# Optimization experiments

Measured on AMD Instinct MI355X. Metric: run time of the kernel, lower is better.

## Reference

```python
import jax, jax.numpy as jnp
import numpy as np

N = 100000      # nodes
E = 1600000     # edges (avg degree 16)
NFEAT = 16
HID = 64
OUT = 4
K = 3           # TAGConv hops
L = 4           # number of TAGConv layers


def setup_inputs() -> dict:
    key = jax.random.key(0)
    ks = jax.random.split(key, 6)
    x = jax.random.normal(ks[0], (N, NFEAT), dtype=jnp.float32)
    edge_index = jax.random.randint(ks[1], (2, E), 0, N, dtype=jnp.int64)
    # TAGConv has one (bias-free) linear per hop k=0..K, plus a per-layer bias.
    W0 = jax.random.normal(ks[2], (K + 1, NFEAT, HID), dtype=jnp.float32) * 0.1
    b0 = jnp.zeros((HID,), dtype=jnp.float32)
    Wh = jax.random.normal(ks[3], (L - 1, K + 1, HID, HID), dtype=jnp.float32) * 0.1
    bh = jnp.zeros((L - 1, HID), dtype=jnp.float32)
    fcW = jax.random.normal(ks[4], (HID, OUT), dtype=jnp.float32) * 0.1
    fcb = jnp.zeros((OUT,), dtype=jnp.float32)
    return dict(x=x, edge_index=edge_index, W0=W0, b0=b0, Wh=Wh, bh=bh, fcW=fcW, fcb=fcb)


def _gcn_norm(src, dst, num_nodes):
    # symmetric GCN normalization, no self-loops (PyG TAGConv default)
    ones = jnp.ones(src.shape, dtype=jnp.float32)
    deg = jax.ops.segment_sum(ones, dst, num_segments=num_nodes)
    dinv = jnp.where(deg > 0, 1.0 / jnp.sqrt(jnp.maximum(deg, 1e-12)), 0.0)
    return dinv[src] * dinv[dst]  # [E]


def _tag_conv(x, src, dst, norm, W, b):
    # out = sum_{k=0..K} (A_norm^k x) W_k + b
    out = x @ W[0]
    h = x
    for k in range(1, W.shape[0]):
        h = jax.ops.segment_sum(norm[:, None] * h[src], dst, num_segments=x.shape[0])
        out = out + h @ W[k]
    return out + b


def reference(x, edge_index, W0, b0, Wh, bh, fcW, fcb):
    src, dst = edge_index[0], edge_index[1]
    norm = _gcn_norm(src, dst, x.shape[0])
    h = jax.nn.relu(_tag_conv(x, src, dst, norm, W0, b0))  # conv0 (+relu, dropout=identity)
    for l in range(Wh.shape[0] - 1):  # middle convs with relu
        h = jax.nn.relu(_tag_conv(h, src, dst, norm, Wh[l], bh[l]))
    h = _tag_conv(h, src, dst, norm, Wh[-1], bh[-1])  # last conv, no relu
    return h @ fcW + fcb  # [N, OUT]
```

## Files before the change

### kernel.cpp

```cpp
#include <hip/hip_runtime.h>
#include <hip/hip_fp16.h>

constexpr int Nn   = 100000;
constexpr int Ne   = 1600000;
constexpr int NF   = 16;
constexpr int HID  = 64;
constexpr int NOUT = 4;

union H8 { float4 f4; __half h[8]; };
union H4 { float2 f2; __half h[4]; };


__global__ __launch_bounds__(256) void hist_kernel(const int* __restrict__ dst,
                                                   int* __restrict__ cnt,
                                                   int* __restrict__ rank) {
    int e = blockIdx.x * 256 + threadIdx.x;
    if (e < Ne) rank[e] = atomicAdd(&cnt[dst[e]], 1);
}

__global__ __launch_bounds__(256) void scan1_kernel(const int* __restrict__ cnt,
                                                    int* __restrict__ rowptr,
                                                    int* __restrict__ bsum) {
    __shared__ int lds[256];
    int t = threadIdx.x;
    int base = blockIdx.x * 1024 + t * 4;
    int v0 = (base + 0 < Nn) ? cnt[base + 0] : 0;
    int v1 = (base + 1 < Nn) ? cnt[base + 1] : 0;
    int v2 = (base + 2 < Nn) ? cnt[base + 2] : 0;
    int v3 = (base + 3 < Nn) ? cnt[base + 3] : 0;
    lds[t] = v0 + v1 + v2 + v3;
    __syncthreads();
    for (int off = 1; off < 256; off <<= 1) {
        int a = lds[t];
        int b = (t >= off) ? lds[t - off] : 0;
        __syncthreads();
        lds[t] = a + b;
        __syncthreads();
    }
    int excl = (t > 0) ? lds[t - 1] : 0;
    if (base + 0 < Nn) rowptr[base + 0] = excl;
    if (base + 1 < Nn) rowptr[base + 1] = excl + v0;
    if (base + 2 < Nn) rowptr[base + 2] = excl + v0 + v1;
    if (base + 3 < Nn) rowptr[base + 3] = excl + v0 + v1 + v2;
    if (t == 255) bsum[blockIdx.x] = lds[255];
}

__global__ __launch_bounds__(128) void scan2_kernel(int* __restrict__ bsum, int nb) {
    __shared__ int lds[128];
    int t = threadIdx.x;
    int v = (t < nb) ? bsum[t] : 0;
    lds[t] = v;
    __syncthreads();
    for (int off = 1; off < 128; off <<= 1) {
        int a = lds[t];
        int b = (t >= off) ? lds[t - off] : 0;
        __syncthreads();
        lds[t] = a + b;
        __syncthreads();
    }
    if (t < nb) bsum[t] = lds[t] - v;
}

__global__ __launch_bounds__(256) void scan3_kernel(const int* __restrict__ cnt,
                                                    int* __restrict__ rowptr,
                                                    const int* __restrict__ bsum,
                                                    float* __restrict__ dinv) {
    int i = blockIdx.x * 256 + threadIdx.x;
    if (i < Nn) {
        rowptr[i] += bsum[i >> 10];
        int c = cnt[i];
        dinv[i] = (c > 0) ? 1.0f / sqrtf((float)c) : 0.0f;
    }
    if (i == 0) rowptr[Nn] = Ne;
}

__global__ __launch_bounds__(256) void scatter_kernel(const int* __restrict__ src,
                                                      const int* __restrict__ dst,
                                                      const int* __restrict__ rowptr,
                                                      const int* __restrict__ rank,
                                                      const float* __restrict__ dinv,
                                                      int2* __restrict__ edge2) {
    int e = blockIdx.x * 256 + threadIdx.x;
    if (e < Ne) {
        int d = dst[e];
        int s = src[e];
        int p = rowptr[d] + rank[e];
        edge2[p] = make_int2(s, __float_as_int(dinv[s]));
    }
}

__global__ __launch_bounds__(256) void xcvt_kernel(const float* __restrict__ x,
                                                   __half* __restrict__ xh) {
    int i = blockIdx.x * 256 + threadIdx.x;
    if (i < Nn * NF / 4) {
        float4 v = reinterpret_cast<const float4*>(x)[i];
        H4 o;
        o.h[0] = __float2half(v.x);
        o.h[1] = __float2half(v.y);
        o.h[2] = __float2half(v.z);
        o.h[3] = __float2half(v.w);
        reinterpret_cast<float2*>(xh)[i] = o.f2;
    }
}


__global__ __launch_bounds__(256) void pull64h_kernel(const __half* __restrict__ hin,
                                                      const int* __restrict__ rowptr,
                                                      const int2* __restrict__ edge2,
                                                      const float* __restrict__ dinv,
                                                      __half* __restrict__ hout) {
    int lane = threadIdx.x & 63;
    int q  = lane & 3;
    int eo = (lane >> 2) & 3;
    int g  = lane >> 4;
    int n = blockIdx.x * 16 + (threadIdx.x >> 6) * 4 + g;
    if (n >= Nn) return;
    int r0 = rowptr[n];
    int r1 = rowptr[n + 1];
    float a[16];
#pragma unroll
    for (int j = 0; j < 16; ++j) a[j] = 0.f;
#pragma unroll 2
    for (int e = r0 + eo; e < r1; e += 4) {
        int2 ed = edge2[e];
        float w = __int_as_float(ed.y);
        const float4* rp = reinterpret_cast<const float4*>(hin + (size_t)ed.x * 64 + q * 16);
        H8 u0, u1;
        u0.f4 = rp[0];
        u1.f4 = rp[1];
#pragma unroll
        for (int j = 0; j < 8; ++j) a[j] += w * __half2float(u0.h[j]);
#pragma unroll
        for (int j = 0; j < 8; ++j) a[8 + j] += w * __half2float(u1.h[j]);
    }
#pragma unroll
    for (int off = 4; off <= 8; off <<= 1)
#pragma unroll
        for (int j = 0; j < 16; ++j) a[j] += __shfl_xor(a[j], off);
    if (eo == 0) {
        float dn = dinv[n];
        H8 o0, o1;
#pragma unroll
        for (int j = 0; j < 8; ++j) o0.h[j] = __float2half(a[j] * dn);
#pragma unroll
        for (int j = 0; j < 8; ++j) o1.h[j] = __float2half(a[8 + j] * dn);
        float4* op = reinterpret_cast<float4*>(hout + (size_t)n * 64 + q * 16);
        op[0] = o0.f4;
        op[1] = o1.f4;
    }
}

__global__ __launch_bounds__(256) void pull16h_kernel(const __half* __restrict__ hin,
                                                      const int* __restrict__ rowptr,
                                                      const int2* __restrict__ edge2,
                                                      const float* __restrict__ dinv,
                                                      __half* __restrict__ hout) {
    int lane = threadIdx.x & 63;
    int q  = lane & 1;
    int eo = (lane >> 1) & 3;
    int g  = lane >> 3;
    int n = blockIdx.x * 32 + (threadIdx.x >> 6) * 8 + g;
    if (n >= Nn) return;
    int r0 = rowptr[n];
    int r1 = rowptr[n + 1];
    float a[8];
#pragma unroll
    for (int j = 0; j < 8; ++j) a[j] = 0.f;
#pragma unroll 2
    for (int e = r0 + eo; e < r1; e += 4) {
        int2 ed = edge2[e];
        float w = __int_as_float(ed.y);
        H8 u;
        u.f4 = *reinterpret_cast<const float4*>(hin + (size_t)ed.x * 16 + q * 8);
#pragma unroll
        for (int j = 0; j < 8; ++j) a[j] += w * __half2float(u.h[j]);
    }
#pragma unroll
    for (int off = 2; off <= 4; off <<= 1)
#pragma unroll
        for (int j = 0; j < 8; ++j) a[j] += __shfl_xor(a[j], off);
    if (eo == 0) {
        float dn = dinv[n];
        H8 o;
#pragma unroll
        for (int j = 0; j < 8; ++j) o.h[j] = __float2half(a[j] * dn);
        *reinterpret_cast<float4*>(hout + (size_t)n * 16 + q * 8) = o.f4;
    }
}

template <int ADDBIAS>
__global__ __launch_bounds__(256) void pull4_kernel(const float* __restrict__ uin,
                                                    const float* __restrict__ gadd,
                                                    const int* __restrict__ rowptr,
                                                    const int2* __restrict__ edge2,
                                                    const float* __restrict__ dinv,
                                                    const float* __restrict__ beff,
                                                    float* __restrict__ out) {
    int lane = threadIdx.x & 63;
    int eo = lane & 15;
    int n = blockIdx.x * 16 + ((threadIdx.x >> 6) << 2) + (lane >> 4);
    if (n >= Nn) return;
    int r0 = rowptr[n];
    int r1 = rowptr[n + 1];
    float ax = 0.f, ay = 0.f, az = 0.f, aw = 0.f;
    for (int e = r0 + eo; e < r1; e += 16) {
        int2 ed = edge2[e];
        float w = __int_as_float(ed.y);
        float4 v = *reinterpret_cast<const float4*>(uin + (size_t)ed.x * 4);
        ax += w * v.x;
        ay += w * v.y;
        az += w * v.z;
        aw += w * v.w;
    }
#pragma unroll
    for (int off = 1; off < 16; off <<= 1) {
        ax += __shfl_xor(ax, off);
        ay += __shfl_xor(ay, off);
        az += __shfl_xor(az, off);
        aw += __shfl_xor(aw, off);
    }
    if (eo == 0) {
        float dn = dinv[n];
        float4 g = *reinterpret_cast<const float4*>(gadd + (size_t)n * 4);
        float4 o;
        o.x = g.x + dn * ax;
        o.y = g.y + dn * ay;
        o.z = g.z + dn * az;
        o.w = g.w + dn * aw;
        if (ADDBIAS) {
            o.x += beff[0]; o.y += beff[1]; o.z += beff[2]; o.w += beff[3];
        }
        *reinterpret_cast<float4*>(out + (size_t)n * 4) = o;
    }
}


template <int KS>
__global__ __launch_bounds__(256) void gemm4_kernel(const __half* __restrict__ S0,
                                                    const __half* __restrict__ S1,
                                                    const __half* __restrict__ S2,
                                                    const __half* __restrict__ S3,
                                                    const float* __restrict__ W,
                                                    const float* __restrict__ bias,
                                                    __half* __restrict__ out) {
    constexpr int PITCH = KS + 4;
    __shared__ float Ht[128 * PITCH];
    __shared__ float Wt[KS * 64];
    int t = threadIdx.x;
    int c4 = t & 15;
    int r8 = t >> 4;
    int r0 = blockIdx.x * 128;
    float acc[8][4];
#pragma unroll
    for (int j = 0; j < 8; ++j)
#pragma unroll
        for (int d = 0; d < 4; ++d) acc[j][d] = 0.f;

    const __half* Ss[4] = {S0, S1, S2, S3};
#pragma unroll
    for (int k = 0; k < 4; ++k) {
        const __half* S = Ss[k];
        for (int i = t; i < KS * 16; i += 256)
            *reinterpret_cast<float4*>(&Wt[i * 4]) =
                *reinterpret_cast<const float4*>(W + (size_t)k * KS * 64 + i * 4);
        for (int i = t; i < 128 * (KS / 8); i += 256) {
            int r = i / (KS / 8);
            int c8 = i % (KS / 8);
            int row = r0 + r;
            float* hp = &Ht[r * PITCH + c8 * 8];
            if (row < Nn) {
                H8 u;
                u.f4 = *reinterpret_cast<const float4*>(S + (size_t)row * KS + c8 * 8);
#pragma unroll
                for (int j = 0; j < 8; ++j) hp[j] = __half2float(u.h[j]);
            } else {
#pragma unroll
                for (int j = 0; j < 8; ++j) hp[j] = 0.f;
            }
        }
        __syncthreads();
#pragma unroll 4
        for (int f = 0; f < KS; ++f) {
            float4 b4 = *reinterpret_cast<const float4*>(&Wt[f * 64 + c4 * 4]);
#pragma unroll
            for (int j = 0; j < 8; ++j) {
                float a = Ht[(r8 + 16 * j) * PITCH + f];
                acc[j][0] += a * b4.x;
                acc[j][1] += a * b4.y;
                acc[j][2] += a * b4.z;
                acc[j][3] += a * b4.w;
            }
        }
        __syncthreads();
    }
    float4 bi = *reinterpret_cast<const float4*>(bias + c4 * 4);
#pragma unroll
    for (int j = 0; j < 8; ++j) {
        int row = r0 + r8 + 16 * j;
        if (row < Nn) {
            H4 o;
            o.h[0] = __float2half(fmaxf(acc[j][0] + bi.x, 0.f));
            o.h[1] = __float2half(fmaxf(acc[j][1] + bi.y, 0.f));
            o.h[2] = __float2half(fmaxf(acc[j][2] + bi.z, 0.f));
            o.h[3] = __float2half(fmaxf(acc[j][3] + bi.w, 0.f));
            *reinterpret_cast<float2*>(out + (size_t)row * 64 + c4 * 4) = o.f2;
        }
    }
}

__global__ __launch_bounds__(256) void weff_kernel(const float* __restrict__ W,
                                                   const float* __restrict__ b,
                                                   const float* __restrict__ fcW,
                                                   const float* __restrict__ fcb,
                                                   float* __restrict__ Wg,
                                                   float* __restrict__ beff) {
    int t = threadIdx.x;
    int k = t >> 6, c = t & 63;
    const float* wrow = W + (size_t)t * 64;
    float a0 = 0.f, a1 = 0.f, a2 = 0.f, a3 = 0.f;
    for (int d = 0; d < 64; ++d) {
        float w = wrow[d];
        a0 += w * fcW[d * 4 + 0];
        a1 += w * fcW[d * 4 + 1];
        a2 += w * fcW[d * 4 + 2];
        a3 += w * fcW[d * 4 + 3];
    }
    float4 o; o.x = a0; o.y = a1; o.z = a2; o.w = a3;
    *reinterpret_cast<float4*>(Wg + k * 256 + c * 4) = o;
    if (t < 4) {
        float s = fcb[t];
        for (int d = 0; d < 64; ++d) s += b[d] * fcW[d * 4 + t];
        beff[t] = s;
    }
}

__global__ __launch_bounds__(256) void gemmG_kernel(const __half* __restrict__ h,
                                                    const float* __restrict__ Wg,
                                                    float* __restrict__ G) {
    __shared__ float Ht[64 * 65];
    __shared__ float Wl[1024];
    int t = threadIdx.x;
    int r0 = blockIdx.x * 64;
    for (int i = t; i < 256; i += 256)
        *reinterpret_cast<float4*>(&Wl[i * 4]) = *reinterpret_cast<const float4*>(Wg + i * 4);
    for (int i = t; i < 64 * 8; i += 256) {
        int r = i >> 3;
        int c8 = i & 7;
        int row = r0 + r;
        float* hp = &Ht[r * 65 + c8 * 8];
        if (row < Nn) {
            H8 u;
            u.f4 = *reinterpret_cast<const float4*>(h + (size_t)row * 64 + c8 * 8);
#pragma unroll
            for (int j = 0; j < 8; ++j) hp[j] = __half2float(u.h[j]);
        } else {
#pragma unroll
            for (int j = 0; j < 8; ++j) hp[j] = 0.f;
        }
    }
    __syncthreads();
    int r = t & 63;
    int k = t >> 6;
    float a0 = 0.f, a1 = 0.f, a2 = 0.f, a3 = 0.f;
#pragma unroll 8
    for (int c = 0; c < 64; ++c) {
        float hv = Ht[r * 65 + c];
        const float* wp = &Wl[k * 256 + c * 4];
        a0 += hv * wp[0];
        a1 += hv * wp[1];
        a2 += hv * wp[2];
        a3 += hv * wp[3];
    }
    int row = r0 + r;
    if (row < Nn) {
        float4 o; o.x = a0; o.y = a1; o.z = a2; o.w = a3;
        *reinterpret_cast<float4*>(G + (size_t)k * Nn * 4 + (size_t)row * 4) = o;
    }
}


extern "C" void kernel_launch(void* const* d_in, const int* in_sizes, int n_in,
                              void* d_out, int out_size, void* d_ws, size_t ws_size,
                              hipStream_t stream) {
    const float* x   = (const float*)d_in[0];
    const int*   ei  = (const int*)d_in[1];
    const float* W0  = (const float*)d_in[2];
    const float* b0  = (const float*)d_in[3];
    const float* Wh  = (const float*)d_in[4];
    const float* bh  = (const float*)d_in[5];
    const float* fcW = (const float*)d_in[6];
    const float* fcb = (const float*)d_in[7];
    float* out = (float*)d_out;

    const int* src = ei;
    const int* dst = ei + Ne;

    int*    rowptr = (int*)d_ws;
    int2*   edge2  = (int2*)(rowptr + 100004);
    int*    rank   = (int*)(rowptr + 100004 + 2 * Ne);
    float*  dinv   = (float*)(rank + Ne);
    int*    bsum   = (int*)(dinv + Nn);
    float*  Wg     = (float*)(bsum + 128);
    float*  beff   = Wg + 1024;
    __half* xh     = (__half*)(beff + 16);
    __half* H0     = xh + (size_t)Nn * NF;
    __half* H1     = H0 + (size_t)Nn * HID;
    __half* H2     = H1 + (size_t)Nn * HID;
    __half* H3     = H2 + (size_t)Nn * HID;
    float*  G      = (float*)(H3 + (size_t)Nn * HID);
    float*  G0     = G + 0 * (size_t)Nn * 4;
    float*  G1     = G + 1 * (size_t)Nn * 4;
    float*  G2     = G + 2 * (size_t)Nn * 4;
    float*  G3     = G + 3 * (size_t)Nn * 4;
    float*  T      = G + 4 * (size_t)Nn * 4;
    float*  T2     = G + 5 * (size_t)Nn * 4;
    int*    cnt    = (int*)(T2 + (size_t)Nn * 4);

    const int egrid  = (Ne + 255) / 256;
    const int ngrid  = (Nn + 255) / 256;
    const int sgrid  = (Nn + 1023) / 1024;
    const int p64grid = (Nn + 15) / 16;
    const int p16grid = (Nn + 31) / 32;
    const int ggrid  = (Nn + 127) / 128;
    const int qgrid  = (Nn + 15) / 16;
    const int Ggrid  = (Nn + 63) / 64;
    const int cgrid  = (Nn * NF / 4 + 255) / 256;

    hipMemsetAsync(cnt, 0, Nn * sizeof(int), stream);
    hist_kernel<<<egrid, 256, 0, stream>>>(dst, cnt, rank);
    scan1_kernel<<<sgrid, 256, 0, stream>>>(cnt, rowptr, bsum);
    scan2_kernel<<<1, 128, 0, stream>>>(bsum, sgrid);
    scan3_kernel<<<ngrid, 256, 0, stream>>>(cnt, rowptr, bsum, dinv);
    scatter_kernel<<<egrid, 256, 0, stream>>>(src, dst, rowptr, rank, dinv, edge2);
    weff_kernel<<<1, 256, 0, stream>>>(Wh + 2 * 4 * 64 * 64, bh + 2 * 64, fcW, fcb, Wg, beff);
    xcvt_kernel<<<cgrid, 256, 0, stream>>>(x, xh);

    pull16h_kernel<<<p16grid, 256, 0, stream>>>(xh, rowptr, edge2, dinv, H1);
    pull16h_kernel<<<p16grid, 256, 0, stream>>>(H1, rowptr, edge2, dinv, H2);
    pull16h_kernel<<<p16grid, 256, 0, stream>>>(H2, rowptr, edge2, dinv, H3);
    gemm4_kernel<NF><<<ggrid, 256, 0, stream>>>(xh, H1, H2, H3, W0, b0, H0);

    for (int l = 0; l < 2; ++l) {
        pull64h_kernel<<<p64grid, 256, 0, stream>>>(H0, rowptr, edge2, dinv, H1);
        pull64h_kernel<<<p64grid, 256, 0, stream>>>(H1, rowptr, edge2, dinv, H2);
        pull64h_kernel<<<p64grid, 256, 0, stream>>>(H2, rowptr, edge2, dinv, H3);
        gemm4_kernel<HID><<<ggrid, 256, 0, stream>>>(H0, H1, H2, H3,
                                                     Wh + (size_t)l * 4 * HID * HID,
                                                     bh + (size_t)l * HID, H0);
    }

    gemmG_kernel<<<Ggrid, 256, 0, stream>>>(H0, Wg, G);
    pull4_kernel<0><<<qgrid, 256, 0, stream>>>(G3, G2, rowptr, edge2, dinv, beff, T);
    pull4_kernel<0><<<qgrid, 256, 0, stream>>>(T,  G1, rowptr, edge2, dinv, beff, T2);
    pull4_kernel<1><<<qgrid, 256, 0, stream>>>(T2, G0, rowptr, edge2, dinv, beff, out);
}
```

Before: 629.9 us.

## Replace atomic-rank CSR build with two-level bucketed counting sort

Builds the CSR by first bucketing edges by dst>>8 with per-chunk LDS histograms and a global scan, scattering (src,dst) pairs into buckets, then sorting each bucket locally in LDS to produce rowptr, dinv and column sources. This replaces the global per-node atomic histogram and the random scatter that used a rank array, aiming to cut global atomic contention and uncoalesced writes. It adds several kernels, extra passes over edge data and a staging buffer aliased onto H1/H2.

```diff
diff --git a/kernel.cpp b/kernel.cpp
--- a/kernel.cpp
+++ b/kernel.cpp
@@ -7,27 +7,39 @@
 constexpr int HID  = 64;
 constexpr int NOUT = 4;
 
+constexpr int NBUK  = 391;
+constexpr int CHUNK = 2048;
+constexpr int NB1   = (Ne + CHUNK - 1) / CHUNK;
+constexpr int NS    = NBUK * NB1;
+constexpr int STASH = 6144;
+
 union H8 { float4 f4; __half h[8]; };
 union H4 { float2 f2; __half h[4]; };
 
 
-__global__ __launch_bounds__(256) void hist_kernel(const int* __restrict__ dst,
-                                                   int* __restrict__ cnt,
-                                                   int* __restrict__ rank) {
-    int e = blockIdx.x * 256 + threadIdx.x;
-    if (e < Ne) rank[e] = atomicAdd(&cnt[dst[e]], 1);
-}
-
-__global__ __launch_bounds__(256) void scan1_kernel(const int* __restrict__ cnt,
-                                                    int* __restrict__ rowptr,
-                                                    int* __restrict__ bsum) {
+__global__ __launch_bounds__(256) void bhist_kernel(const int* __restrict__ dst,
+                                                    int* __restrict__ ghist) {
+    __shared__ int h[NBUK];
+    int t = threadIdx.x;
+    int b = blockIdx.x;
+    for (int i = t; i < NBUK; i += 256) h[i] = 0;
+    __syncthreads();
+    int e0 = b * CHUNK;
+    int e1 = (e0 + CHUNK < Ne) ? e0 + CHUNK : Ne;
+    for (int e = e0 + t; e < e1; e += 256) atomicAdd(&h[dst[e] >> 8], 1);
+    __syncthreads();
+    for (int i = t; i < NBUK; i += 256) ghist[i * NB1 + b] = h[i];
+}
+
+__global__ __launch_bounds__(256) void scan1g_kernel(int* __restrict__ g,
+                                                     int* __restrict__ bsum) {
     __shared__ int lds[256];
     int t = threadIdx.x;
     int base = blockIdx.x * 1024 + t * 4;
-    int v0 = (base + 0 < Nn) ? cnt[base + 0] : 0;
-    int v1 = (base + 1 < Nn) ? cnt[base + 1] : 0;
-    int v2 = (base + 2 < Nn) ? cnt[base + 2] : 0;
-    int v3 = (base + 3 < Nn) ? cnt[base + 3] : 0;
+    int v0 = (base + 0 < NS) ? g[base + 0] : 0;
+    int v1 = (base + 1 < NS) ? g[base + 1] : 0;
+    int v2 = (base + 2 < NS) ? g[base + 2] : 0;
+    int v3 = (base + 3 < NS) ? g[base + 3] : 0;
     lds[t] = v0 + v1 + v2 + v3;
     __syncthreads();
     for (int off = 1; off < 256; off <<= 1) {
@@ -38,20 +50,20 @@
         __syncthreads();
     }
     int excl = (t > 0) ? lds[t - 1] : 0;
-    if (base + 0 < Nn) rowptr[base + 0] = excl;
-    if (base + 1 < Nn) rowptr[base + 1] = excl + v0;
-    if (base + 2 < Nn) rowptr[base + 2] = excl + v0 + v1;
-    if (base + 3 < Nn) rowptr[base + 3] = excl + v0 + v1 + v2;
+    if (base + 0 < NS) g[base + 0] = excl;
+    if (base + 1 < NS) g[base + 1] = excl + v0;
+    if (base + 2 < NS) g[base + 2] = excl + v0 + v1;
+    if (base + 3 < NS) g[base + 3] = excl + v0 + v1 + v2;
     if (t == 255) bsum[blockIdx.x] = lds[255];
 }
 
-__global__ __launch_bounds__(128) void scan2_kernel(int* __restrict__ bsum, int nb) {
-    __shared__ int lds[128];
+__global__ __launch_bounds__(512) void scan2g_kernel(int* __restrict__ bsum, int nb) {
+    __shared__ int lds[512];
     int t = threadIdx.x;
     int v = (t < nb) ? bsum[t] : 0;
     lds[t] = v;
     __syncthreads();
-    for (int off = 1; off < 128; off <<= 1) {
+    for (int off = 1; off < 512; off <<= 1) {
         int a = lds[t];
         int b = (t >= off) ? lds[t - off] : 0;
         __syncthreads();
@@ -61,31 +73,94 @@
     if (t < nb) bsum[t] = lds[t] - v;
 }
 
-__global__ __launch_bounds__(256) void scan3_kernel(const int* __restrict__ cnt,
-                                                    int* __restrict__ rowptr,
-                                                    const int* __restrict__ bsum,
-                                                    float* __restrict__ dinv) {
+__global__ __launch_bounds__(256) void scan3g_kernel(int* __restrict__ g,
+                                                     const int* __restrict__ bsum) {
     int i = blockIdx.x * 256 + threadIdx.x;
-    if (i < Nn) {
-        rowptr[i] += bsum[i >> 10];
-        int c = cnt[i];
-        dinv[i] = (c > 0) ? 1.0f / sqrtf((float)c) : 0.0f;
-    }
-    if (i == 0) rowptr[Nn] = Ne;
-}
-
-__global__ __launch_bounds__(256) void scatter_kernel(const int* __restrict__ src,
-                                                      const int* __restrict__ dst,
-                                                      const int* __restrict__ rowptr,
-                                                      const int* __restrict__ rank,
-                                                      const float* __restrict__ dinv,
-                                                      int2* __restrict__ edge2) {
+    if (i < NS) g[i] += bsum[i >> 10];
+}
+
+__global__ __launch_bounds__(256) void bscatter_kernel(const int* __restrict__ src,
+                                                       const int* __restrict__ dst,
+                                                       const int* __restrict__ ghist,
+                                                       int2* __restrict__ tmp) {
+    __shared__ int hb[NBUK];
+    __shared__ int cur[NBUK];
+    int t = threadIdx.x;
+    int b = blockIdx.x;
+    for (int i = t; i < NBUK; i += 256) {
+        hb[i] = ghist[i * NB1 + b];
+        cur[i] = 0;
+    }
+    __syncthreads();
+    int e0 = b * CHUNK;
+    int e1 = (e0 + CHUNK < Ne) ? e0 + CHUNK : Ne;
+    for (int e = e0 + t; e < e1; e += 256) {
+        int d = dst[e];
+        int s = src[e];
+        int bin = d >> 8;
+        int r = atomicAdd(&cur[bin], 1);
+        tmp[hb[bin] + r] = make_int2(s, d);
+    }
+}
+
+__global__ __launch_bounds__(256) void bcsr_kernel(const int2* __restrict__ tmp,
+                                                   const int* __restrict__ ghist,
+                                                   int* __restrict__ rowptr,
+                                                   float* __restrict__ dinv,
+                                                   int* __restrict__ colsrc) {
+    __shared__ int2 stash[STASH];
+    __shared__ int h[256];
+    __shared__ int hs[256];
+    __shared__ int cur[256];
+    int t = threadIdx.x;
+    int b = blockIdx.x;
+    int lo = ghist[b * NB1];
+    int hi = (b < NBUK - 1) ? ghist[(b + 1) * NB1] : Ne;
+    int sz = hi - lo;
+    h[t] = 0;
+    cur[t] = 0;
+    __syncthreads();
+    for (int i = t; i < sz; i += 256) {
+        int2 rec = tmp[lo + i];
+        if (i < STASH) stash[i] = rec;
+        atomicAdd(&h[rec.y & 255], 1);
+    }
+    __syncthreads();
+    int myh = h[t];
+    hs[t] = myh;
+    __syncthreads();
+    for (int off = 1; off < 256; off <<= 1) {
+        int a = hs[t];
+        int bb = (t >= off) ? hs[t - off] : 0;
+        __syncthreads();
+        hs[t] = a + bb;
+        __syncthreads();
+    }
+    int excl = hs[t] - myh;
+    __syncthreads();
+    hs[t] = excl;
+    int d = (b << 8) + t;
+    if (d < Nn) {
+        rowptr[d] = lo + excl;
+        dinv[d] = (myh > 0) ? rsqrtf((float)myh) : 0.0f;
+    }
+    if (b == NBUK - 1 && t == 0) rowptr[Nn] = Ne;
+    __syncthreads();
+    for (int i = t; i < sz; i += 256) {
+        int2 rec = (i < STASH) ? stash[i] : tmp[lo + i];
+        int bin = rec.y & 255;
+        int r = atomicAdd(&cur[bin], 1);
+        colsrc[lo + hs[bin] + r] = rec.x;
+    }
+}
+
+__global__ __launch_bounds__(256) void fill_kernel(const int* __restrict__ colsrc,
+                                                   const float* __restrict__ dinv,
+                                                   int2* __restrict__ edge2) {
     int e = blockIdx.x * 256 + threadIdx.x;
     if (e < Ne) {
-        int d = dst[e];
-        int s = src[e];
-        int p = rowptr[d] + rank[e];
-        edge2[p] = make_int2(s, __float_as_int(dinv[s]));
+        int s = colsrc[e];
+        edge2[e] = make_int2(s, __float_as_int(dinv[s]));
     }
 }
 
@@ -397,10 +472,10 @@
 
     int*    rowptr = (int*)d_ws;
     int2*   edge2  = (int2*)(rowptr + 100004);
-    int*    rank   = (int*)(rowptr + 100004 + 2 * Ne);
-    float*  dinv   = (float*)(rank + Ne);
-    int*    bsum   = (int*)(dinv + Nn);
-    float*  Wg     = (float*)(bsum + 128);
+    int*    ghist  = (int*)(rowptr + 100004 + 2 * Ne);
+    int*    bsum   = ghist + 305792;
+    float*  dinv   = (float*)(bsum + 512);
+    float*  Wg     = dinv + Nn;
     float*  beff   = Wg + 1024;
     __half* xh     = (__half*)(beff + 16);
     __half* H0     = xh + (size_t)Nn * NF;
@@ -414,11 +489,12 @@
     float*  G3     = G + 3 * (size_t)Nn * 4;
     float*  T      = G + 4 * (size_t)Nn * 4;
     float*  T2     = G + 5 * (size_t)Nn * 4;
-    int*    cnt    = (int*)(T2 + (size_t)Nn * 4);
+    int2*   tmp    = (int2*)H2;
+    int*    colsrc = (int*)H1;
 
     const int egrid  = (Ne + 255) / 256;
-    const int ngrid  = (Nn + 255) / 256;
-    const int sgrid  = (Nn + 1023) / 1024;
+    const int s1grid = (NS + 1023) / 1024;
+    const int s3grid = (NS + 255) / 256;
     const int p64grid = (Nn + 15) / 16;
     const int p16grid = (Nn + 31) / 32;
     const int ggrid  = (Nn + 127) / 128;
@@ -426,12 +502,13 @@
     const int Ggrid  = (Nn + 63) / 64;
     const int cgrid  = (Nn * NF / 4 + 255) / 256;
 
-    hipMemsetAsync(cnt, 0, Nn * sizeof(int), stream);
-    hist_kernel<<<egrid, 256, 0, stream>>>(dst, cnt, rank);
-    scan1_kernel<<<sgrid, 256, 0, stream>>>(cnt, rowptr, bsum);
-    scan2_kernel<<<1, 128, 0, stream>>>(bsum, sgrid);
-    scan3_kernel<<<ngrid, 256, 0, stream>>>(cnt, rowptr, bsum, dinv);
-    scatter_kernel<<<egrid, 256, 0, stream>>>(src, dst, rowptr, rank, dinv, edge2);
+    bhist_kernel<<<NB1, 256, 0, stream>>>(dst, ghist);
+    scan1g_kernel<<<s1grid, 256, 0, stream>>>(ghist, bsum);
+    scan2g_kernel<<<1, 512, 0, stream>>>(bsum, s1grid);
+    scan3g_kernel<<<s3grid, 256, 0, stream>>>(ghist, bsum);
+    bscatter_kernel<<<NB1, 256, 0, stream>>>(src, dst, ghist, tmp);
+    bcsr_kernel<<<NBUK, 256, 0, stream>>>(tmp, ghist, rowptr, dinv, colsrc);
+    fill_kernel<<<egrid, 256, 0, stream>>>(colsrc, dinv, edge2);
     weff_kernel<<<1, 256, 0, stream>>>(Wh + 2 * 4 * 64 * 64, bh + 2 * 64, fcW, fcb, Wg, beff);
     xcvt_kernel<<<cgrid, 256, 0, stream>>>(x, xh);
 
```

New measurement: 592.1 us. -6.0%, faster.
